# Kernel tuning notes

Hardware: AMD Instinct MI355X
Metric: run time of the kernel (lower is better)

Reference implementation:

```python
import math
import jax, jax.numpy as jnp
import numpy as np

N_HEADS = 16
D_EMBED = 1024

def setup_inputs() -> dict:
    key = jax.random.key(0)
    ks = jax.random.split(key, 5)
    b, l, d = 2, 2048, D_EMBED
    return {
        "x": jax.random.normal(ks[0], (b, l, d), dtype=jnp.float32),
        "w_in": jax.random.normal(ks[1], (3 * d, d), dtype=jnp.float32) * 0.02,
        "b_in": jax.random.normal(ks[2], (3 * d,), dtype=jnp.float32) * 0.02,
        "w_out": jax.random.normal(ks[3], (d, d), dtype=jnp.float32) * 0.02,
        "b_out": jax.random.normal(ks[4], (d,), dtype=jnp.float32) * 0.02,
    }

def reference(x, w_in, b_in, w_out, b_out):
    b, l, d = x.shape
    h = N_HEADS
    scale = 1.0 / math.sqrt(d // h)
    # in_proj then reshape to heads BEFORE chunking (faithful to source:
    # each head's 3*d_head block is split into q/k/v)
    x_proj = (x @ w_in.T + b_in).reshape(b, l, h, -1)  # (b,l,h,3*dh)
    q, k, v = jnp.split(x_proj, 3, axis=-1)            # each (b,l,h,dh)
    att = jnp.einsum('blhd,bmhd->blmh', q, k) * scale  # (b,l,m,h)
    # causal_mask=False path of the original forward
    att = jax.nn.softmax(att, axis=2)                  # softmax over keys m
    # faithful to source einsum 'blmh, blhd-> blhd' (sums att over m against
    # v indexed by l, exactly as the original code computes)
    opt = jnp.einsum('blmh,blhd->blhd', att, v).reshape(b, l, d)
    return opt @ w_out.T + b_out
```

## Files before the change

kernel.cpp:

```cpp
#include <hip/hip_runtime.h>

typedef unsigned short ushort_t;
typedef __bf16 bf16x8 __attribute__((ext_vector_type(8)));
typedef float f32x4 __attribute__((ext_vector_type(4)));

static __device__ __forceinline__ ushort_t f2bf(float f) {
    __bf16 b = (__bf16)f;
    return __builtin_bit_cast(ushort_t, b);
}

#define GLOAD_LDS16(gptr, lptr)                                                        \
    __builtin_amdgcn_global_load_lds(                                                  \
        (const __attribute__((address_space(1))) void*)(gptr),                         \
        (__attribute__((address_space(3))) void*)(lptr), 16, 0, 0)

#define CFENCE() asm volatile("" ::: "memory")

template <int N> __device__ __forceinline__ void waitcnt_vm() {
    if constexpr (N == 0)      asm volatile("s_waitcnt vmcnt(0)" ::: "memory");
    else if constexpr (N == 2) asm volatile("s_waitcnt vmcnt(2)" ::: "memory");
    else if constexpr (N == 4) asm volatile("s_waitcnt vmcnt(4)" ::: "memory");
    else if constexpr (N == 8) asm volatile("s_waitcnt vmcnt(8)" ::: "memory");
}

template <int BM, int BN, int WGM, int WGN, bool BF16_OUT>
__device__ __forceinline__
void gemm_core(const ushort_t* __restrict__ A, const ushort_t* __restrict__ B,
               const float* __restrict__ bias, void* __restrict__ C,
               const int K, const int N, const int rA, const int rB,
               ushort_t* ls) {
    constexpr int WM = BM / WGM, WN = BN / WGN;
    constexpr int MI = WM / 16, NJ = WN / 16;
    constexpr int LA = (BM * 32) / (8 * 256);
    constexpr int LB = (BN * 32) / (8 * 256);
    constexpr int L  = LA + LB;
    constexpr int HALF = (BM + BN) * 32;

    const int tid  = threadIdx.x;
    const int lane = tid & 63;
    const int wv   = tid >> 6;
    const int wr   = wv / WGN, wc = wv % WGN;
    const int fr   = lane & 15, fq = lane >> 4;

    f32x4 acc[MI][NJ] = {};

    auto stage = [&](int k0, int buf) {
        #pragma unroll
        for (int q = 0; q < LA; ++q) {
            int c = q * 256 + tid;
            GLOAD_LDS16(A + (size_t)(rA + (c >> 2)) * K + k0 + (c & 3) * 8,
                        &ls[buf * HALF + c * 8]);
        }
        #pragma unroll
        for (int q = 0; q < LB; ++q) {
            int c = q * 256 + tid;
            GLOAD_LDS16(B + (size_t)(rB + (c >> 2)) * K + k0 + (c & 3) * 8,
                        &ls[buf * HALF + BM * 32 + c * 8]);
        }
    };

    auto compute = [&](int buf) {
        bf16x8 af[MI], bfv[NJ];
        #pragma unroll
        for (int i = 0; i < MI; ++i)
            af[i] = *(const bf16x8*)&ls[buf * HALF + (wr * WM + i * 16 + fr) * 32 + fq * 8];
        #pragma unroll
        for (int j = 0; j < NJ; ++j)
            bfv[j] = *(const bf16x8*)&ls[buf * HALF + BM * 32 + (wc * WN + j * 16 + fr) * 32 + fq * 8];
        #pragma unroll
        for (int i = 0; i < MI; ++i)
            #pragma unroll
            for (int j = 0; j < NJ; ++j)
                acc[i][j] = __builtin_amdgcn_mfma_f32_16x16x32_bf16(af[i], bfv[j], acc[i][j], 0, 0, 0);
    };

    const int T = K >> 5;
    stage(0, 0);
    stage(32, 1);
    int cur = 0, nxt2 = 2;
    for (int t = 0; t < T - 2; ++t) {
        stage((t + 2) << 5, nxt2);
        waitcnt_vm<2 * L>();
        __builtin_amdgcn_s_barrier(); CFENCE();
        compute(cur);
        CFENCE(); __builtin_amdgcn_s_barrier(); CFENCE();
        cur  = (cur  + 1 == 3) ? 0 : cur  + 1;
        nxt2 = (nxt2 + 1 == 3) ? 0 : nxt2 + 1;
    }
    waitcnt_vm<L>();
    __builtin_amdgcn_s_barrier(); CFENCE();
    compute(cur);
    cur = (cur + 1 == 3) ? 0 : cur + 1;
    CFENCE();
    waitcnt_vm<0>();
    __builtin_amdgcn_s_barrier(); CFENCE();
    compute(cur);

    const int orow0 = rA + wr * WM + fq * 4;
    const int ocol0 = rB + wc * WN + fr;
    #pragma unroll
    for (int i = 0; i < MI; ++i)
        #pragma unroll
        for (int j = 0; j < NJ; ++j) {
            const int col = ocol0 + j * 16;
            const float bv = bias ? bias[col] : 0.f;
            #pragma unroll
            for (int r = 0; r < 4; ++r) {
                const int row = orow0 + i * 16 + r;
                const float v = acc[i][j][r] + bv;
                if constexpr (BF16_OUT)
                    ((ushort_t*)C)[(size_t)row * N + col] = f2bf(v);
                else
                    ((float*)C)[(size_t)row * N + col] = v;
            }
        }
}

__global__ __launch_bounds__(256)
void prep(const float* __restrict__ w_in, const float* __restrict__ b_in,
          const float* __restrict__ w_out, const float* __restrict__ b_out,
          ushort_t* __restrict__ wob, ushort_t* __restrict__ Pt,
          float* __restrict__ bfused) {
    __shared__ ushort_t tile[64][65];
    const int b = blockIdx.x;
    const int t = threadIdx.x;

    if (b < 128) {
        #pragma unroll
        for (int p = 0; p < 8; ++p) {
            int i = b * 2048 + p * 256 + t;
            float4 v = ((const float4*)w_out)[i];
            ushort4 o; o.x = f2bf(v.x); o.y = f2bf(v.y); o.z = f2bf(v.z); o.w = f2bf(v.w);
            ((ushort4*)wob)[i] = o;
        }
    } else if (b < 384) {
        const int g = b - 128;
        const int gx = g & 15, gy = g >> 4;
        #pragma unroll
        for (int p = 0; p < 16; ++p) {
            int e = p * 256 + t;
            int j = e >> 6, c = e & 63;
            tile[j][c] = f2bf(w_in[(size_t)(gx * 192 + 128 + j) * 1024 + gy * 64 + c]);
        }
        __syncthreads();
        #pragma unroll
        for (int p = 0; p < 16; ++p) {
            int e = p * 256 + t;
            int c = e >> 6, j = e & 63;
            Pt[(size_t)(gy * 64 + c) * 1024 + gx * 64 + j] = tile[j][c];
        }
    } else {
        const int w = t >> 6, lane = t & 63;
        const int row = (b - 384) * 4 + w;
        float s = 0.f;
        #pragma unroll
        for (int it = 0; it < 16; ++it) {
            int j = it * 64 + lane;
            int r = (j >> 6) * 192 + 128 + (j & 63);
            s += w_out[(size_t)row * 1024 + j] * b_in[r];
        }
        #pragma unroll
        for (int off = 32; off; off >>= 1) s += __shfl_down(s, off, 64);
        if (lane == 0) bfused[row] = s + b_out[row];
    }
}

__global__ __launch_bounds__(256)
void k2(const ushort_t* __restrict__ wob, const ushort_t* __restrict__ Pt,
        ushort_t* __restrict__ Wfb,
        const float* __restrict__ x, ushort_t* __restrict__ xb) {
    __shared__ alignas(16) ushort_t ls[3 * (64 + 64) * 32];
    const int b = blockIdx.x;
    if (b < 256) {
        const int swz = (b & 7) * 32 + (b >> 3);
        const int by = swz >> 4, bx = swz & 15;
        gemm_core<64, 64, 2, 2, true>(wob, Pt, nullptr, (void*)Wfb, 1024, 1024,
                                      by * 64, bx * 64, ls);
    } else {
        const int g = b - 256;
        const int t = threadIdx.x;
        #pragma unroll
        for (int p = 0; p < 8; ++p) {
            int i = g * 2048 + p * 256 + t;
            float4 v = ((const float4*)x)[i];
            ushort4 o; o.x = f2bf(v.x); o.y = f2bf(v.y); o.z = f2bf(v.z); o.w = f2bf(v.w);
            ((ushort4*)xb)[i] = o;
        }
    }
}

__global__ __launch_bounds__(256)
void k3(const ushort_t* __restrict__ xb, const ushort_t* __restrict__ Wfb,
        const float* __restrict__ bfused, float* __restrict__ out) {
    __shared__ alignas(16) ushort_t ls[3 * (128 + 128) * 32];
    const int b = blockIdx.x;
    const int swz = (b & 7) * 32 + (b >> 3);
    const int by = swz >> 3, bx = swz & 7;
    gemm_core<128, 128, 2, 2, false>(xb, Wfb, bfused, (void*)out, 1024, 1024,
                                     by * 128, bx * 128, ls);
}

extern "C" void kernel_launch(void* const* d_in, const int* in_sizes, int n_in,
                              void* d_out, int out_size, void* d_ws, size_t ws_size,
                              hipStream_t stream) {
    const float* x     = (const float*)d_in[0];
    const float* w_in  = (const float*)d_in[1];
    const float* b_in  = (const float*)d_in[2];
    const float* w_out = (const float*)d_in[3];
    const float* b_out = (const float*)d_in[4];
    float* out = (float*)d_out;

    char* ws = (char*)d_ws;
    ushort_t* xb     = (ushort_t*)(ws);
    ushort_t* wob    = (ushort_t*)(ws + (8u  << 20));
    ushort_t* Pt     = (ushort_t*)(ws + (10u << 20));
    ushort_t* Wfb    = (ushort_t*)(ws + (12u << 20));
    float*    bfused = (float*)   (ws + (14u << 20));

    prep<<<640, 256, 0, stream>>>(w_in, b_in, w_out, b_out, wob, Pt, bfused);
    k2<<<768, 256, 0, stream>>>(wob, Pt, Wfb, x, xb);
    k3<<<256, 256, 0, stream>>>(xb, Wfb, bfused, out);
}
```

Before: 37.23 us.

## Replace fused-weight GEMM with two chained GEMMs and in-loop x conversion

Stops precomputing the fused weight Wo·Wv and its transposed Wv copy. Instead it computes V = x·Wv^T + b_v in a first GEMM, then out = V·Wo^T + b_out in a second. The first GEMM reads fp32 x directly and converts it to bf16 in registers before writing LDS, removing the separate x-cast pass and the bias-fusion reduction. This trades a small 1024^3 GEMM for a second full-size 4096x1024x1024 GEMM, raising total FLOPs, and the register-staged A path may pipeline less well than the async LDS loads.

```diff
diff --git a/kernel.cpp b/kernel.cpp
--- a/kernel.cpp
+++ b/kernel.cpp
@@ -3,6 +3,7 @@
 typedef unsigned short ushort_t;
 typedef __bf16 bf16x8 __attribute__((ext_vector_type(8)));
 typedef float f32x4 __attribute__((ext_vector_type(4)));
+typedef ushort_t ushort8 __attribute__((ext_vector_type(8)));
 
 static __device__ __forceinline__ ushort_t f2bf(float f) {
     __bf16 b = (__bf16)f;
@@ -15,6 +16,7 @@
         (__attribute__((address_space(3))) void*)(lptr), 16, 0, 0)
 
 #define CFENCE() asm volatile("" ::: "memory")
+#define LGKM0()  asm volatile("s_waitcnt lgkmcnt(0)" ::: "memory")
 
 template <int N> __device__ __forceinline__ void waitcnt_vm() {
     if constexpr (N == 0)      asm volatile("s_waitcnt vmcnt(0)" ::: "memory");
@@ -23,108 +25,193 @@
     else if constexpr (N == 8) asm volatile("s_waitcnt vmcnt(8)" ::: "memory");
 }
 
-template <int BM, int BN, int WGM, int WGN, bool BF16_OUT>
-__device__ __forceinline__
-void gemm_core(const ushort_t* __restrict__ A, const ushort_t* __restrict__ B,
-               const float* __restrict__ bias, void* __restrict__ C,
-               const int K, const int N, const int rA, const int rB,
-               ushort_t* ls) {
-    constexpr int WM = BM / WGM, WN = BN / WGN;
-    constexpr int MI = WM / 16, NJ = WN / 16;
-    constexpr int LA = (BM * 32) / (8 * 256);
-    constexpr int LB = (BN * 32) / (8 * 256);
-    constexpr int L  = LA + LB;
-    constexpr int HALF = (BM + BN) * 32;
+__global__ __launch_bounds__(256)
+void gemm_a(const float* __restrict__ A32, const ushort_t* __restrict__ B,
+            const float* __restrict__ b_in, ushort_t* __restrict__ V) {
+    constexpr int K = 1024, N = 1024, T = 32;
+    constexpr int ABUF = 128 * 32, BBUF = 128 * 32;
+    __shared__ alignas(16) ushort_t ls[3 * (ABUF + BBUF)];
+    ushort_t* Ab = ls;
+    ushort_t* Bb = ls + 3 * ABUF;
+
+    const int b = blockIdx.x;
+    const int swz = (b & 7) * 32 + (b >> 3);
+    const int rA = (swz >> 3) * 128, rB = (swz & 7) * 128;
 
     const int tid  = threadIdx.x;
     const int lane = tid & 63;
     const int wv   = tid >> 6;
-    const int wr   = wv / WGN, wc = wv % WGN;
+    const int wr   = wv >> 1, wc = wv & 1;
     const int fr   = lane & 15, fq = lane >> 4;
 
-    f32x4 acc[MI][NJ] = {};
+    const int ar = tid >> 2;
+    const int ac = (tid & 3) * 8;
+
+    f32x4 acc[4][4] = {};
+    float4 areg[4];
+
+    auto aload = [&](int k0) {
+        const float* p0 = A32 + (size_t)(rA + ar) * K + k0 + ac;
+        const float* p1 = A32 + (size_t)(rA + ar + 64) * K + k0 + ac;
+        areg[0] = ((const float4*)p0)[0]; areg[1] = ((const float4*)p0)[1];
+        areg[2] = ((const float4*)p1)[0]; areg[3] = ((const float4*)p1)[1];
+    };
+    auto awrite = [&](int buf) {
+        ushort8 lo, hi;
+        lo[0]=f2bf(areg[0].x); lo[1]=f2bf(areg[0].y); lo[2]=f2bf(areg[0].z); lo[3]=f2bf(areg[0].w);
+        lo[4]=f2bf(areg[1].x); lo[5]=f2bf(areg[1].y); lo[6]=f2bf(areg[1].z); lo[7]=f2bf(areg[1].w);
+        hi[0]=f2bf(areg[2].x); hi[1]=f2bf(areg[2].y); hi[2]=f2bf(areg[2].z); hi[3]=f2bf(areg[2].w);
+        hi[4]=f2bf(areg[3].x); hi[5]=f2bf(areg[3].y); hi[6]=f2bf(areg[3].z); hi[7]=f2bf(areg[3].w);
+        *(ushort8*)&Ab[buf * ABUF + ar * 32 + ac]        = lo;
+        *(ushort8*)&Ab[buf * ABUF + (ar + 64) * 32 + ac] = hi;
+    };
+    auto bstage = [&](int k0, int buf) {
+        #pragma unroll
+        for (int q = 0; q < 2; ++q) {
+            int c = q * 256 + tid;
+            GLOAD_LDS16(B + (size_t)(rB + (c >> 2)) * K + k0 + (c & 3) * 8,
+                        &Bb[buf * BBUF + c * 8]);
+        }
+    };
+    auto compute = [&](int buf) {
+        bf16x8 af[4], bfv[4];
+        #pragma unroll
+        for (int i = 0; i < 4; ++i)
+            af[i] = *(const bf16x8*)&Ab[buf * ABUF + (wr * 64 + i * 16 + fr) * 32 + fq * 8];
+        #pragma unroll
+        for (int j = 0; j < 4; ++j)
+            bfv[j] = *(const bf16x8*)&Bb[buf * BBUF + (wc * 64 + j * 16 + fr) * 32 + fq * 8];
+        #pragma unroll
+        for (int i = 0; i < 4; ++i)
+            #pragma unroll
+            for (int j = 0; j < 4; ++j)
+                acc[i][j] = __builtin_amdgcn_mfma_f32_16x16x32_bf16(af[i], bfv[j], acc[i][j], 0, 0, 0);
+    };
+
+    bstage(0, 0);
+    aload(0);
+    bstage(32, 1);
+    awrite(0);
+    aload(32);
+    LGKM0();
+    __builtin_amdgcn_s_barrier(); CFENCE();
+
+    for (int t = 0; t < T - 2; ++t) {
+        const int cur = t % 3, nx1 = (t + 1) % 3, nx2 = (t + 2) % 3;
+        bstage((t + 2) << 5, nx2);
+        compute(cur);
+        awrite(nx1);
+        aload((t + 2) << 5);
+        LGKM0();
+        CFENCE(); __builtin_amdgcn_s_barrier(); CFENCE();
+    }
+    {
+        const int cur = (T - 2) % 3, nx1 = (T - 1) % 3;
+        compute(cur);
+        awrite(nx1);
+        LGKM0();
+        CFENCE(); __builtin_amdgcn_s_barrier(); CFENCE();
+        compute(nx1);
+    }
+
+    const int orow0 = rA + wr * 64 + fq * 4;
+    const int ocol0 = rB + wc * 64 + fr;
+    #pragma unroll
+    for (int i = 0; i < 4; ++i)
+        #pragma unroll
+        for (int j = 0; j < 4; ++j) {
+            const int col = ocol0 + j * 16;
+            const float bv = b_in[(col >> 6) * 192 + 128 + (col & 63)];
+            #pragma unroll
+            for (int r = 0; r < 4; ++r)
+                V[(size_t)(orow0 + i * 16 + r) * N + col] = f2bf(acc[i][j][r] + bv);
+        }
+}
+
+__global__ __launch_bounds__(256)
+void gemm_b(const ushort_t* __restrict__ A, const ushort_t* __restrict__ B,
+            const float* __restrict__ bias, float* __restrict__ C) {
+    constexpr int K = 1024, N = 1024, T = 32;
+    constexpr int HALF = 256 * 32;
+    __shared__ alignas(16) ushort_t ls[3 * HALF];
+
+    const int b = blockIdx.x;
+    const int swz = (b & 7) * 32 + (b >> 3);
+    const int rA = (swz >> 3) * 128, rB = (swz & 7) * 128;
+
+    const int tid  = threadIdx.x;
+    const int lane = tid & 63;
+    const int wv   = tid >> 6;
+    const int wr   = wv >> 1, wc = wv & 1;
+    const int fr   = lane & 15, fq = lane >> 4;
+
+    f32x4 acc[4][4] = {};
 
     auto stage = [&](int k0, int buf) {
         #pragma unroll
-        for (int q = 0; q < LA; ++q) {
+        for (int q = 0; q < 2; ++q) {
             int c = q * 256 + tid;
             GLOAD_LDS16(A + (size_t)(rA + (c >> 2)) * K + k0 + (c & 3) * 8,
                         &ls[buf * HALF + c * 8]);
         }
         #pragma unroll
-        for (int q = 0; q < LB; ++q) {
+        for (int q = 0; q < 2; ++q) {
             int c = q * 256 + tid;
             GLOAD_LDS16(B + (size_t)(rB + (c >> 2)) * K + k0 + (c & 3) * 8,
-                        &ls[buf * HALF + BM * 32 + c * 8]);
-        }
-    };
-
+                        &ls[buf * HALF + 4096 + c * 8]);
+        }
+    };
     auto compute = [&](int buf) {
-        bf16x8 af[MI], bfv[NJ];
-        #pragma unroll
-        for (int i = 0; i < MI; ++i)
-            af[i] = *(const bf16x8*)&ls[buf * HALF + (wr * WM + i * 16 + fr) * 32 + fq * 8];
-        #pragma unroll
-        for (int j = 0; j < NJ; ++j)
-            bfv[j] = *(const bf16x8*)&ls[buf * HALF + BM * 32 + (wc * WN + j * 16 + fr) * 32 + fq * 8];
-        #pragma unroll
-        for (int i = 0; i < MI; ++i)
-            #pragma unroll
-            for (int j = 0; j < NJ; ++j)
+        bf16x8 af[4], bfv[4];
+        #pragma unroll
+        for (int i = 0; i < 4; ++i)
+            af[i] = *(const bf16x8*)&ls[buf * HALF + (wr * 64 + i * 16 + fr) * 32 + fq * 8];
+        #pragma unroll
+        for (int j = 0; j < 4; ++j)
+            bfv[j] = *(const bf16x8*)&ls[buf * HALF + 4096 + (wc * 64 + j * 16 + fr) * 32 + fq * 8];
+        #pragma unroll
+        for (int i = 0; i < 4; ++i)
+            #pragma unroll
+            for (int j = 0; j < 4; ++j)
                 acc[i][j] = __builtin_amdgcn_mfma_f32_16x16x32_bf16(af[i], bfv[j], acc[i][j], 0, 0, 0);
     };
 
-    const int T = K >> 5;
     stage(0, 0);
     stage(32, 1);
-    int cur = 0, nxt2 = 2;
     for (int t = 0; t < T - 2; ++t) {
-        stage((t + 2) << 5, nxt2);
-        waitcnt_vm<2 * L>();
+        stage((t + 2) << 5, (t + 2) % 3);
+        waitcnt_vm<8>();
         __builtin_amdgcn_s_barrier(); CFENCE();
-        compute(cur);
+        compute(t % 3);
         CFENCE(); __builtin_amdgcn_s_barrier(); CFENCE();
-        cur  = (cur  + 1 == 3) ? 0 : cur  + 1;
-        nxt2 = (nxt2 + 1 == 3) ? 0 : nxt2 + 1;
-    }
-    waitcnt_vm<L>();
+    }
+    waitcnt_vm<4>();
     __builtin_amdgcn_s_barrier(); CFENCE();
-    compute(cur);
-    cur = (cur + 1 == 3) ? 0 : cur + 1;
+    compute((T - 2) % 3);
     CFENCE();
     waitcnt_vm<0>();
     __builtin_amdgcn_s_barrier(); CFENCE();
-    compute(cur);
-
-    const int orow0 = rA + wr * WM + fq * 4;
-    const int ocol0 = rB + wc * WN + fr;
+    compute((T - 1) % 3);
+
+    const int orow0 = rA + wr * 64 + fq * 4;
+    const int ocol0 = rB + wc * 64 + fr;
     #pragma unroll
-    for (int i = 0; i < MI; ++i)
-        #pragma unroll
-        for (int j = 0; j < NJ; ++j) {
+    for (int i = 0; i < 4; ++i)
+        #pragma unroll
+        for (int j = 0; j < 4; ++j) {
             const int col = ocol0 + j * 16;
-            const float bv = bias ? bias[col] : 0.f;
-            #pragma unroll
-            for (int r = 0; r < 4; ++r) {
-                const int row = orow0 + i * 16 + r;
-                const float v = acc[i][j][r] + bv;
-                if constexpr (BF16_OUT)
-                    ((ushort_t*)C)[(size_t)row * N + col] = f2bf(v);
-                else
-                    ((float*)C)[(size_t)row * N + col] = v;
-            }
+            const float bv = bias[col];
+            #pragma unroll
+            for (int r = 0; r < 4; ++r)
+                C[(size_t)(orow0 + i * 16 + r) * N + col] = acc[i][j][r] + bv;
         }
 }
 
 __global__ __launch_bounds__(256)
-void prep(const float* __restrict__ w_in, const float* __restrict__ b_in,
-          const float* __restrict__ w_out, const float* __restrict__ b_out,
-          ushort_t* __restrict__ wob, ushort_t* __restrict__ Pt,
-          float* __restrict__ bfused) {
-    __shared__ ushort_t tile[64][65];
+void prep(const float* __restrict__ w_in, const float* __restrict__ w_out,
+          ushort_t* __restrict__ wob, ushort_t* __restrict__ Wvb) {
     const int b = blockIdx.x;
     const int t = threadIdx.x;
-
     if (b < 128) {
         #pragma unroll
         for (int p = 0; p < 8; ++p) {
@@ -133,71 +220,20 @@
             ushort4 o; o.x = f2bf(v.x); o.y = f2bf(v.y); o.z = f2bf(v.z); o.w = f2bf(v.w);
             ((ushort4*)wob)[i] = o;
         }
-    } else if (b < 384) {
-        const int g = b - 128;
-        const int gx = g & 15, gy = g >> 4;
-        #pragma unroll
-        for (int p = 0; p < 16; ++p) {
-            int e = p * 256 + t;
-            int j = e >> 6, c = e & 63;
-            tile[j][c] = f2bf(w_in[(size_t)(gx * 192 + 128 + j) * 1024 + gy * 64 + c]);
-        }
-        __syncthreads();
-        #pragma unroll
-        for (int p = 0; p < 16; ++p) {
-            int e = p * 256 + t;
-            int c = e >> 6, j = e & 63;
-            Pt[(size_t)(gy * 64 + c) * 1024 + gx * 64 + j] = tile[j][c];
-        }
     } else {
-        const int w = t >> 6, lane = t & 63;
-        const int row = (b - 384) * 4 + w;
-        float s = 0.f;
-        #pragma unroll
-        for (int it = 0; it < 16; ++it) {
-            int j = it * 64 + lane;
-            int r = (j >> 6) * 192 + 128 + (j & 63);
-            s += w_out[(size_t)row * 1024 + j] * b_in[r];
-        }
-        #pragma unroll
-        for (int off = 32; off; off >>= 1) s += __shfl_down(s, off, 64);
-        if (lane == 0) bfused[row] = s + b_out[row];
-    }
-}
-
-__global__ __launch_bounds__(256)
-void k2(const ushort_t* __restrict__ wob, const ushort_t* __restrict__ Pt,
-        ushort_t* __restrict__ Wfb,
-        const float* __restrict__ x, ushort_t* __restrict__ xb) {
-    __shared__ alignas(16) ushort_t ls[3 * (64 + 64) * 32];
-    const int b = blockIdx.x;
-    if (b < 256) {
-        const int swz = (b & 7) * 32 + (b >> 3);
-        const int by = swz >> 4, bx = swz & 15;
-        gemm_core<64, 64, 2, 2, true>(wob, Pt, nullptr, (void*)Wfb, 1024, 1024,
-                                      by * 64, bx * 64, ls);
-    } else {
-        const int g = b - 256;
-        const int t = threadIdx.x;
-        #pragma unroll
-        for (int p = 0; p < 8; ++p) {
-            int i = g * 2048 + p * 256 + t;
-            float4 v = ((const float4*)x)[i];
+        const int j = (b - 128) * 4 + (t >> 6);
+        const int lane = t & 63;
+        const int r = (j >> 6) * 192 + 128 + (j & 63);
+        const float4* src = (const float4*)(w_in + (size_t)r * 1024);
+        ushort4* dst = (ushort4*)(Wvb + (size_t)j * 1024);
+        #pragma unroll
+        for (int k = 0; k < 4; ++k) {
+            int i = k * 64 + lane;
+            float4 v = src[i];
             ushort4 o; o.x = f2bf(v.x); o.y = f2bf(v.y); o.z = f2bf(v.z); o.w = f2bf(v.w);
-            ((ushort4*)xb)[i] = o;
-        }
-    }
-}
-
-__global__ __launch_bounds__(256)
-void k3(const ushort_t* __restrict__ xb, const ushort_t* __restrict__ Wfb,
-        const float* __restrict__ bfused, float* __restrict__ out) {
-    __shared__ alignas(16) ushort_t ls[3 * (128 + 128) * 32];
-    const int b = blockIdx.x;
-    const int swz = (b & 7) * 32 + (b >> 3);
-    const int by = swz >> 3, bx = swz & 7;
-    gemm_core<128, 128, 2, 2, false>(xb, Wfb, bfused, (void*)out, 1024, 1024,
-                                     by * 128, bx * 128, ls);
+            dst[i] = o;
+        }
+    }
 }
 
 extern "C" void kernel_launch(void* const* d_in, const int* in_sizes, int n_in,
@@ -211,13 +247,11 @@
     float* out = (float*)d_out;
 
     char* ws = (char*)d_ws;
-    ushort_t* xb     = (ushort_t*)(ws);
-    ushort_t* wob    = (ushort_t*)(ws + (8u  << 20));
-    ushort_t* Pt     = (ushort_t*)(ws + (10u << 20));
-    ushort_t* Wfb    = (ushort_t*)(ws + (12u << 20));
-    float*    bfused = (float*)   (ws + (14u << 20));
-
-    prep<<<640, 256, 0, stream>>>(w_in, b_in, w_out, b_out, wob, Pt, bfused);
-    k2<<<768, 256, 0, stream>>>(wob, Pt, Wfb, x, xb);
-    k3<<<256, 256, 0, stream>>>(xb, Wfb, bfused, out);
-}
+    ushort_t* wob = (ushort_t*)(ws);
+    ushort_t* Wvb = (ushort_t*)(ws + (2u << 20));
+    ushort_t* Vb  = (ushort_t*)(ws + (4u << 20));
+
+    prep<<<384, 256, 0, stream>>>(w_in, w_out, wob, Wvb);
+    gemm_a<<<256, 256, 0, stream>>>(x, Wvb, b_in, Vb);
+    gemm_b<<<256, 256, 0, stream>>>(Vb, wob, b_out, out);
+}
```

Measured after the change: 48.10 us. 29.2% more time.
